# Kernel tuning notes

Measured on AMD Instinct MI355X. Metric: run time of the kernel, lower is better.

The kernel has to match this reference:

```python
import jax, jax.numpy as jnp
import numpy as np

N = 50000      # nodes
E = 800000     # edges (before self-loops)
C_IN = 128
HID = 128
C_OUT = 64
B = 64         # graphs in batch
NEG_SLOPE = 0.2
EPS = 1e-16


def setup_inputs() -> dict:
    key = jax.random.key(0)
    ks = jax.random.split(key, 12)
    x = jax.random.normal(ks[0], (N, C_IN), dtype=jnp.float32)
    edge_index = jax.random.randint(ks[1], (2, E), 0, N, dtype=jnp.int64)
    batch = jnp.sort(jax.random.randint(ks[2], (N,), 0, B, dtype=jnp.int64))
    g1 = 1.0 / np.sqrt(C_IN)
    g2 = 1.0 / np.sqrt(HID)
    return {
        'x': x,
        'edge_index': edge_index,
        'batch': batch,
        'W1': jax.random.normal(ks[3], (C_IN, HID), jnp.float32) * g1,
        'a_src1': jax.random.normal(ks[4], (HID,), jnp.float32) * g2,
        'a_dst1': jax.random.normal(ks[5], (HID,), jnp.float32) * g2,
        'b1': jnp.zeros((HID,), jnp.float32),
        'W2': jax.random.normal(ks[6], (HID, C_OUT), jnp.float32) * g2,
        'a_src2': jax.random.normal(ks[7], (C_OUT,), jnp.float32) / np.sqrt(C_OUT),
        'a_dst2': jax.random.normal(ks[8], (C_OUT,), jnp.float32) / np.sqrt(C_OUT),
        'b2': jnp.zeros((C_OUT,), jnp.float32),
    }


def _gat_conv(x, src, dst, W, a_src, a_dst, b):
    # PyG GATConv, heads=1, self-loops already appended to (src, dst).
    h = x @ W                                   # [N, F]
    alpha = h[src] @ a_src + h[dst] @ a_dst     # [E'] per-edge logit
    alpha = jax.nn.leaky_relu(alpha, NEG_SLOPE)
    # segment softmax over incoming edges of each destination node
    amax = jax.ops.segment_max(alpha, dst, num_segments=N)
    e = jnp.exp(alpha - amax[dst])
    denom = jax.ops.segment_sum(e, dst, num_segments=N)
    att = e / (denom[dst] + EPS)                # [E']
    out = jax.ops.segment_sum(att[:, None] * h[src], dst, num_segments=N)
    return out + b


def reference(x, edge_index, batch, W1, a_src1, a_dst1, b1, W2, a_src2, a_dst2, b2):
    loop = jnp.arange(N, dtype=edge_index.dtype)
    src = jnp.concatenate([edge_index[0], loop])  # add_self_loops=True
    dst = jnp.concatenate([edge_index[1], loop])
    h = _gat_conv(x, src, dst, W1, a_src1, a_dst1, b1)
    h = jax.nn.relu(h)
    h = _gat_conv(h, src, dst, W2, a_src2, a_dst2, b2)
    # global mean pool over graph ids
    sums = jax.ops.segment_sum(h, batch, num_segments=B)          # [B, C_OUT]
    cnt = jax.ops.segment_sum(jnp.ones((N,), h.dtype), batch, num_segments=B)
    pooled = sums / jnp.maximum(cnt, 1.0)[:, None]
    return jax.nn.log_softmax(pooled, axis=1)
```

## Files before the change

### kernel.cpp

```cpp
#include <hip/hip_runtime.h>
#include <math.h>

#define NN 50000
#define EE 800000
#define EP (EE + NN)
#define COUT 64
#define BB 64
#define NEG_SLOPE 0.2f
#define EPSF 1e-16f
#define NPART 8
#define PNODES (NN / NPART)
#define CAPE 128
#define GM 782

typedef unsigned short u16;
typedef __attribute__((ext_vector_type(8))) short bf16x8;
typedef __attribute__((ext_vector_type(4))) float f32x4;

__device__ __forceinline__ u16 f2b(float f) {
    union { float f; unsigned u; } v; v.f = f;
    unsigned u = v.u;
    return (u16)((u + 0x7FFFu + ((u >> 16) & 1u)) >> 16);
}
__device__ __forceinline__ float b2f(u16 h) {
    union { unsigned u; float f; } v; v.u = ((unsigned)h) << 16;
    return v.f;
}
__device__ __forceinline__ float leaky(float v) {
    return (v > 0.f) ? v : NEG_SLOPE * v;
}

__global__ __launch_bounds__(256) void k_pre(const float* __restrict__ W1,
                                             const float* __restrict__ W2,
                                             u16* __restrict__ W1t,
                                             u16* __restrict__ W2t,
                                             int* __restrict__ deg,
                                             float* __restrict__ sums) {
    int b = blockIdx.x;
    if (b < 96) {
        int t = b * 256 + threadIdx.x;
        if (t < 128 * 128) {
            int c = t >> 7, k = t & 127;
            W1t[t] = f2b(W1[k * 128 + c]);
        } else {
            int o = t - 128 * 128;
            int c = o >> 7, k = o & 127;
            W2t[o] = f2b(W2[k * 64 + c]);
        }
    } else {
        int n = (b - 96) * 256 + threadIdx.x;
        if (n < NN) deg[n] = 0;
        if (n < BB * COUT) sums[n] = 0.f;
    }
}

__global__ __launch_bounds__(256) void k_scatter(const int* __restrict__ src,
                                                 const int* __restrict__ dst,
                                                 int* __restrict__ deg,
                                                 u16* __restrict__ col_ell) {
    int v = blockIdx.x & (NPART - 1);
    int cid = blockIdx.x >> 3;
    int nchunk = gridDim.x >> 3;
    int lo = v * PNODES, hi = lo + PNODES;
    for (int e = cid * 256 + threadIdx.x; e < EP; e += nchunk * 256) {
        int dd = (e < EE) ? dst[e] : (e - EE);
        if (dd >= lo && dd < hi) {
            int s = (e < EE) ? src[e] : dd;
            int pos = atomicAdd(&deg[dd], 1);
            if (pos < CAPE) col_ell[(size_t)dd * CAPE + pos] = (u16)s;
        }
    }
}

template <int F, bool ABF16>
__device__ __forceinline__ void gemm_body(int bx,
                                          const void* __restrict__ Xv,
                                          const u16* __restrict__ Wt,
                                          u16* __restrict__ H,
                                          const float* __restrict__ a_src,
                                          const float* __restrict__ a_dst,
                                          float* __restrict__ sdot,
                                          float* __restrict__ ddot) {
    __shared__ u16 Ab[64 * 128];
    __shared__ u16 Bb[F * 128];
    int tid = threadIdx.x;
    int row0 = bx * 64;

    if (ABF16) {
        const u16* X = (const u16*)Xv;
        #pragma unroll
        for (int it = 0; it < 4; it++) {
            int c = it * 256 + tid;
            int row = c >> 4;
            int k8 = (c & 15) * 8;
            int grow = row0 + row;
            uint4 val = {0u, 0u, 0u, 0u};
            if (grow < NN) val = *(const uint4*)&X[(size_t)grow * 128 + k8];
            *(uint4*)&Ab[row * 128 + (k8 ^ ((row & 7) << 3))] = val;
        }
    } else {
        const float* X = (const float*)Xv;
        #pragma unroll
        for (int it = 0; it < 8; it++) {
            int c = it * 256 + tid;
            int e = c * 4;
            int row = e >> 7;
            int col = e & 127;
            int grow = row0 + row;
            float4 v = {0.f, 0.f, 0.f, 0.f};
            if (grow < NN) v = *(const float4*)&X[(size_t)grow * 128 + col];
            ushort4 o;
            o.x = f2b(v.x); o.y = f2b(v.y); o.z = f2b(v.z); o.w = f2b(v.w);
            *(ushort4*)&Ab[row * 128 + (col ^ ((row & 7) << 3))] = o;
        }
    }
    const int NB = F * 128 / 8 / 256;
    #pragma unroll
    for (int it = 0; it < NB; it++) {
        int c = it * 256 + tid;
        int col = c >> 4;
        int k8 = (c & 15) * 8;
        uint4 val = *(const uint4*)&Wt[col * 128 + k8];
        *(uint4*)&Bb[col * 128 + (k8 ^ ((col & 7) << 3))] = val;
    }
    __syncthreads();

    int w = tid >> 6, l = tid & 63;
    int g = l >> 4;
    int rA = l & 15;
    const int NT = F / 16;
    f32x4 acc[NT];
    #pragma unroll
    for (int ct = 0; ct < NT; ct++) {
        acc[ct][0] = 0.f; acc[ct][1] = 0.f; acc[ct][2] = 0.f; acc[ct][3] = 0.f;
    }
    int arow = w * 16 + rA;
    int abase = arow * 128;
    int sw = (rA & 7) << 3;
    #pragma unroll
    for (int ks = 0; ks < 4; ks++) {
        int koff = ks * 32 + g * 8;
        bf16x8 af = *(const bf16x8*)&Ab[abase + (koff ^ sw)];
        #pragma unroll
        for (int ct = 0; ct < NT; ct++) {
            int bcol = ct * 16 + rA;
            bf16x8 bfv = *(const bf16x8*)&Bb[bcol * 128 + (koff ^ sw)];
            acc[ct] = __builtin_amdgcn_mfma_f32_16x16x32_bf16(af, bfv, acc[ct], 0, 0, 0);
        }
    }

    float asv[NT], adv[NT];
    #pragma unroll
    for (int ct = 0; ct < NT; ct++) {
        asv[ct] = a_src[ct * 16 + rA];
        adv[ct] = a_dst[ct * 16 + rA];
    }
    float ps[4] = {0.f, 0.f, 0.f, 0.f};
    float pd[4] = {0.f, 0.f, 0.f, 0.f};
    #pragma unroll
    for (int ct = 0; ct < NT; ct++) {
        #pragma unroll
        for (int r = 0; r < 4; r++) {
            ps[r] += acc[ct][r] * asv[ct];
            pd[r] += acc[ct][r] * adv[ct];
        }
    }
    #pragma unroll
    for (int r = 0; r < 4; r++) {
        int grow = row0 + w * 16 + g * 4 + r;
        if (grow < NN) {
            #pragma unroll
            for (int ct = 0; ct < NT; ct++) {
                H[(size_t)grow * F + ct * 16 + rA] = f2b(acc[ct][r]);
            }
        }
    }
    #pragma unroll
    for (int r = 0; r < 4; r++) {
        #pragma unroll
        for (int off = 1; off < 16; off <<= 1) {
            ps[r] += __shfl_xor(ps[r], off);
            pd[r] += __shfl_xor(pd[r], off);
        }
    }
    if (rA == 0) {
        #pragma unroll
        for (int r = 0; r < 4; r++) {
            int grow = row0 + w * 16 + g * 4 + r;
            if (grow < NN) { sdot[grow] = ps[r]; ddot[grow] = pd[r]; }
        }
    }
}

__global__ __launch_bounds__(256) void k_gemm1(const float* __restrict__ x,
                                               const u16* __restrict__ W1t,
                                               u16* __restrict__ h1,
                                               const float* __restrict__ as1,
                                               const float* __restrict__ ad1,
                                               float* __restrict__ s1,
                                               float* __restrict__ d1) {
    gemm_body<128, false>(blockIdx.x, x, W1t, h1, as1, ad1, s1, d1);
}

__global__ __launch_bounds__(256) void k_gemm2(const u16* __restrict__ x2,
                                               const u16* __restrict__ W2t,
                                               u16* __restrict__ h2,
                                               const float* __restrict__ as2,
                                               const float* __restrict__ ad2,
                                               float* __restrict__ s2,
                                               float* __restrict__ d2) {
    gemm_body<64, true>(blockIdx.x, x2, W2t, h2, as2, ad2, s2, d2);
}

template <int ROWB>
__device__ __forceinline__ float stage_weights(const u16* __restrict__ colrow,
                                               const float* __restrict__ s,
                                               float dn, int deg, int lane,
                                               float* __restrict__ wl,
                                               int* __restrict__ wc) {
    float M = -INFINITY;
    for (int e0 = 0; e0 < deg; e0 += 64) {
        int e = e0 + lane;
        float l = -INFINITY; int c = 0;
        if (e < deg) { c = colrow[e]; l = leaky(s[c] + dn); }
        wl[e0 + lane] = l;
        wc[e0 + lane] = c * ROWB;
        float cm = l;
        #pragma unroll
        for (int off = 32; off; off >>= 1) cm = fmaxf(cm, __shfl_xor(cm, off));
        M = fmaxf(M, cm);
    }
    float Sl = 0.f;
    for (int i0 = 0; i0 < deg; i0 += 64) {
        float u = __expf(wl[i0 + lane] - M);
        wl[i0 + lane] = u;
        Sl += u;
    }
    #pragma unroll
    for (int off = 32; off; off >>= 1) Sl += __shfl_xor(Sl, off);
    return 1.f / (Sl + EPSF);
}

__global__ __launch_bounds__(256) void k_fused1(const int* __restrict__ degv,
                                                const u16* __restrict__ col_ell,
                                                const float* __restrict__ s,
                                                const float* __restrict__ d,
                                                const u16* __restrict__ H,
                                                const float* __restrict__ bias,
                                                u16* __restrict__ outb) {
    const int F = 128;
    __shared__ float wl[4][CAPE];
    __shared__ int   wc[4][CAPE];
    int w = threadIdx.x >> 6;
    int lane = threadIdx.x & 63;
    int n = blockIdx.x * 4 + w;
    if (n >= NN) return;
    int deg = degv[n];
    if (deg > CAPE) deg = CAPE;
    const u16* colrow = col_ell + (size_t)n * CAPE;
    float dn = d[n];
    const char* Hb = (const char*)H + lane * 4;
    float2 acc = {0.f, 0.f};

    float invS = stage_weights<F * 2>(colrow, s, dn, deg, lane, wl[w], wc[w]);
    int i = 0;
    for (; i + 8 <= deg; i += 8) {
        float u0 = wl[w][i+0], u1 = wl[w][i+1], u2 = wl[w][i+2], u3 = wl[w][i+3];
        float u4 = wl[w][i+4], u5 = wl[w][i+5], u6 = wl[w][i+6], u7 = wl[w][i+7];
        int o0 = wc[w][i+0], o1 = wc[w][i+1], o2 = wc[w][i+2], o3 = wc[w][i+3];
        int o4 = wc[w][i+4], o5 = wc[w][i+5], o6 = wc[w][i+6], o7 = wc[w][i+7];
        ushort2 r0 = *(const ushort2*)(Hb + o0);
        ushort2 r1 = *(const ushort2*)(Hb + o1);
        ushort2 r2 = *(const ushort2*)(Hb + o2);
        ushort2 r3 = *(const ushort2*)(Hb + o3);
        ushort2 r4 = *(const ushort2*)(Hb + o4);
        ushort2 r5 = *(const ushort2*)(Hb + o5);
        ushort2 r6 = *(const ushort2*)(Hb + o6);
        ushort2 r7 = *(const ushort2*)(Hb + o7);
        acc.x += u0 * b2f(r0.x); acc.y += u0 * b2f(r0.y);
        acc.x += u1 * b2f(r1.x); acc.y += u1 * b2f(r1.y);
        acc.x += u2 * b2f(r2.x); acc.y += u2 * b2f(r2.y);
        acc.x += u3 * b2f(r3.x); acc.y += u3 * b2f(r3.y);
        acc.x += u4 * b2f(r4.x); acc.y += u4 * b2f(r4.y);
        acc.x += u5 * b2f(r5.x); acc.y += u5 * b2f(r5.y);
        acc.x += u6 * b2f(r6.x); acc.y += u6 * b2f(r6.y);
        acc.x += u7 * b2f(r7.x); acc.y += u7 * b2f(r7.y);
    }
    for (; i < deg; ++i) {
        float u = wl[w][i];
        ushort2 r = *(const ushort2*)(Hb + wc[w][i]);
        acc.x += u * b2f(r.x); acc.y += u * b2f(r.y);
    }
    float2 b = *(const float2*)&bias[lane * 2];
    acc.x = fmaxf(acc.x * invS + b.x, 0.f);
    acc.y = fmaxf(acc.y * invS + b.y, 0.f);
    ushort2 o; o.x = f2b(acc.x); o.y = f2b(acc.y);
    *(ushort2*)&outb[(size_t)n * F + lane * 2] = o;
}

#define NPW 4
__global__ __launch_bounds__(256) void k_fused2(const int* __restrict__ degv,
                                                const u16* __restrict__ col_ell,
                                                const float* __restrict__ s,
                                                const float* __restrict__ d,
                                                const u16* __restrict__ H,
                                                const float* __restrict__ bias,
                                                const int* __restrict__ batch,
                                                float* __restrict__ sums) {
    const int F = 64;
    __shared__ float wl[4][CAPE];
    __shared__ int   wc[4][CAPE];
    int wave = threadIdx.x >> 6;
    int lane = threadIdx.x & 63;
    int base = (blockIdx.x * 4 + wave) * NPW;
    int lim = base + NPW;
    float bs = bias[lane];
    const char* Hb = (const char*)H + lane * 2;
    float gacc = 0.f;
    int gb = batch[base];

    for (int n = base; n < lim; ++n) {
        int b = batch[n];
        if (b != gb) {
            atomicAdd(&sums[gb * COUT + lane], gacc);
            gacc = 0.f; gb = b;
        }
        int deg = degv[n];
        if (deg > CAPE) deg = CAPE;
        const u16* colrow = col_ell + (size_t)n * CAPE;
        float dn = d[n];
        float acc = 0.f;

        float invS = stage_weights<F * 2>(colrow, s, dn, deg, lane, wl[wave], wc[wave]);
        int i = 0;
        for (; i + 8 <= deg; i += 8) {
            float u0 = wl[wave][i+0], u1 = wl[wave][i+1], u2 = wl[wave][i+2], u3 = wl[wave][i+3];
            float u4 = wl[wave][i+4], u5 = wl[wave][i+5], u6 = wl[wave][i+6], u7 = wl[wave][i+7];
            int o0 = wc[wave][i+0], o1 = wc[wave][i+1], o2 = wc[wave][i+2], o3 = wc[wave][i+3];
            int o4 = wc[wave][i+4], o5 = wc[wave][i+5], o6 = wc[wave][i+6], o7 = wc[wave][i+7];
            u16 r0 = *(const u16*)(Hb + o0); u16 r1 = *(const u16*)(Hb + o1);
            u16 r2 = *(const u16*)(Hb + o2); u16 r3 = *(const u16*)(Hb + o3);
            u16 r4 = *(const u16*)(Hb + o4); u16 r5 = *(const u16*)(Hb + o5);
            u16 r6 = *(const u16*)(Hb + o6); u16 r7 = *(const u16*)(Hb + o7);
            acc += u0 * b2f(r0) + u1 * b2f(r1) + u2 * b2f(r2) + u3 * b2f(r3);
            acc += u4 * b2f(r4) + u5 * b2f(r5) + u6 * b2f(r6) + u7 * b2f(r7);
        }
        for (; i < deg; ++i) {
            acc += wl[wave][i] * b2f(*(const u16*)(Hb + wc[wave][i]));
        }
        gacc += acc * invS + bs;
    }
    atomicAdd(&sums[gb * COUT + lane], gacc);
}

__global__ __launch_bounds__(256) void k_logsm(const float* __restrict__ sums,
                                               const int* __restrict__ batch,
                                               float* __restrict__ out) {
    int wave = threadIdx.x >> 6;
    int lane = threadIdx.x & 63;
    int g = blockIdx.x * 4 + wave;
    if (g >= BB) return;
    int lo = 0, hi = NN;
    while (lo < hi) { int mid = (lo + hi) >> 1; if (batch[mid] < g) lo = mid + 1; else hi = mid; }
    int l2 = lo, h2 = NN;
    while (l2 < h2) { int mid = (l2 + h2) >> 1; if (batch[mid] < g + 1) l2 = mid + 1; else h2 = mid; }
    float cnt = (float)(h2 - lo);
    float mean = sums[g * COUT + lane] / fmaxf(cnt, 1.f);
    float mx = mean;
    #pragma unroll
    for (int off = 32; off; off >>= 1) mx = fmaxf(mx, __shfl_xor(mx, off));
    float ex = __expf(mean - mx);
    float sm = ex;
    #pragma unroll
    for (int off = 32; off; off >>= 1) sm += __shfl_xor(sm, off);
    out[g * COUT + lane] = mean - mx - logf(sm);
}

extern "C" void kernel_launch(void* const* d_in, const int* in_sizes, int n_in,
                              void* d_out, int out_size, void* d_ws, size_t ws_size,
                              hipStream_t stream) {
    const float* x      = (const float*)d_in[0];
    const int*   eidx   = (const int*)d_in[1];
    const int*   batch  = (const int*)d_in[2];
    const float* W1     = (const float*)d_in[3];
    const float* a_src1 = (const float*)d_in[4];
    const float* a_dst1 = (const float*)d_in[5];
    const float* b1     = (const float*)d_in[6];
    const float* W2     = (const float*)d_in[7];
    const float* a_src2 = (const float*)d_in[8];
    const float* a_dst2 = (const float*)d_in[9];
    const float* b2     = (const float*)d_in[10];
    float* out = (float*)d_out;

    const int* src = eidx;
    const int* dst = eidx + EE;

    char* w = (char*)d_ws;
    auto alloc = [&](size_t bytes) { void* p = (void*)w; w += (bytes + 255) & ~(size_t)255; return p; };
    float* sums  = (float*)alloc((size_t)BB * COUT * 4);
    float* s1    = (float*)alloc((size_t)NN * 4);
    float* d1    = (float*)alloc((size_t)NN * 4);
    float* s2    = (float*)alloc((size_t)NN * 4);
    float* d2    = (float*)alloc((size_t)NN * 4);
    int* deg     = (int*)alloc((size_t)NN * 4);
    u16* col_ell = (u16*)alloc((size_t)NN * CAPE * 2);
    u16* h1      = (u16*)alloc((size_t)NN * 128 * 2);
    u16* x2      = (u16*)alloc((size_t)NN * 128 * 2);
    u16* h2      = (u16*)alloc((size_t)NN * 64 * 2);
    u16* W1t     = (u16*)alloc((size_t)128 * 128 * 2);
    u16* W2t     = (u16*)alloc((size_t)64 * 128 * 2);

    dim3 blk(256);
    int gN4 = (NN + 3) / 4;

    k_pre<<<292, blk, 0, stream>>>(W1, W2, W1t, W2t, deg, sums);
    k_scatter<<<4096, blk, 0, stream>>>(src, dst, deg, col_ell);

    k_gemm1<<<GM, blk, 0, stream>>>(x, W1t, h1, a_src1, a_dst1, s1, d1);
    k_fused1<<<gN4, blk, 0, stream>>>(deg, col_ell, s1, d1, h1, b1, x2);

    k_gemm2<<<GM, blk, 0, stream>>>(x2, W2t, h2, a_src2, a_dst2, s2, d2);
    k_fused2<<<NN / (4 * NPW), blk, 0, stream>>>(deg, col_ell, s2, d2, h2, b2, batch, sums);

    k_logsm<<<(BB + 3) / 4, blk, 0, stream>>>(sums, batch, out);
}
```

Before: 150.3 us.

## Split layer-1 attention into weight kernel and channel-sliced gather kernel

Layer-1 aggregation is split in two. A new kernel computes the normalized softmax weights per edge and stores them as bf16 in an ELL array. The gather kernel then runs four times as many blocks, each handling a 32-channel slice with four edge groups per wave, and reduces the partial sums with shuffles. This is meant to increase parallelism and memory-level parallelism in the gather. The cost is an extra launch, extra global traffic for the weight array, and bf16 rounding of the attention weights.

Result: slower. 190.6 us (+26.9%).

```diff
diff --git a/kernel.cpp b/kernel.cpp
--- a/kernel.cpp
+++ b/kernel.cpp
@@ -12,6 +12,7 @@
 #define PNODES (NN / NPART)
 #define CAPE 128
 #define GM 782
+#define NSL 4
 
 typedef unsigned short u16;
 typedef __attribute__((ext_vector_type(8))) short bf16x8;
@@ -25,6 +26,12 @@
 __device__ __forceinline__ float b2f(u16 h) {
     union { unsigned u; float f; } v; v.u = ((unsigned)h) << 16;
     return v.f;
+}
+__device__ __forceinline__ float lo16(unsigned v) {
+    union { unsigned u; float f; } x; x.u = v << 16; return x.f;
+}
+__device__ __forceinline__ float hi16(unsigned v) {
+    union { unsigned u; float f; } x; x.u = v & 0xffff0000u; return x.f;
 }
 __device__ __forceinline__ float leaky(float v) {
     return (v > 0.f) ? v : NEG_SLOPE * v;
@@ -212,6 +219,105 @@
     gemm_body<64, true>(blockIdx.x, x2, W2t, h2, as2, ad2, s2, d2);
 }
 
+__global__ __launch_bounds__(256) void k_weights(const int* __restrict__ degv,
+                                                 const u16* __restrict__ col_ell,
+                                                 const float* __restrict__ s,
+                                                 const float* __restrict__ d,
+                                                 u16* __restrict__ w_ell) {
+    __shared__ float wl[4][CAPE];
+    int w = threadIdx.x >> 6;
+    int lane = threadIdx.x & 63;
+    int n = blockIdx.x * 4 + w;
+    int deg = degv[n];
+    if (deg > CAPE) deg = CAPE;
+    const u16* colrow = col_ell + (size_t)n * CAPE;
+    float dn = d[n];
+
+    float M = -INFINITY;
+    for (int e0 = 0; e0 < deg; e0 += 64) {
+        int e = e0 + lane;
+        float l = -INFINITY;
+        if (e < deg) l = leaky(s[colrow[e]] + dn);
+        wl[w][e0 + lane] = l;
+        float cm = l;
+        #pragma unroll
+        for (int off = 32; off; off >>= 1) cm = fmaxf(cm, __shfl_xor(cm, off));
+        M = fmaxf(M, cm);
+    }
+    float Sl = 0.f;
+    for (int i0 = 0; i0 < deg; i0 += 64) {
+        float u = __expf(wl[w][i0 + lane] - M);
+        wl[w][i0 + lane] = u;
+        Sl += u;
+    }
+    #pragma unroll
+    for (int off = 32; off; off >>= 1) Sl += __shfl_xor(Sl, off);
+    float invS = 1.f / (Sl + EPSF);
+
+    int degC = (deg + 63) & ~63;
+    for (int i0 = 0; i0 < degC; i0 += 64) {
+        w_ell[(size_t)n * CAPE + i0 + lane] = f2b(wl[w][i0 + lane] * invS);
+    }
+}
+
+__global__ __launch_bounds__(256) void k_fused1(const int* __restrict__ degv,
+                                                const u16* __restrict__ col_ell,
+                                                const u16* __restrict__ w_ell,
+                                                const u16* __restrict__ H,
+                                                const float* __restrict__ bias,
+                                                u16* __restrict__ outb) {
+    const int F = 128;
+    __shared__ float wl[4][CAPE];
+    __shared__ int   off[4][CAPE];
+    int w = threadIdx.x >> 6;
+    int lane = threadIdx.x & 63;
+    int c = blockIdx.x & (NSL - 1);
+    int n = (blockIdx.x >> 2) * 4 + w;
+    int deg = degv[n];
+    if (deg > CAPE) deg = CAPE;
+    int degR = (deg + 31) & ~31;
+
+    {
+        float wf = (lane < degR) ? b2f(w_ell[(size_t)n * CAPE + lane]) : 0.f;
+        int   of = (lane < deg) ? ((int)col_ell[(size_t)n * CAPE + lane] << 8) : 0;
+        wl[w][lane] = wf;
+        off[w][lane] = of;
+        if (degR > 64) {
+            int e = 64 + lane;
+            wl[w][e] = (e < degR) ? b2f(w_ell[(size_t)n * CAPE + e]) : 0.f;
+            off[w][e] = (e < deg) ? ((int)col_ell[(size_t)n * CAPE + e] << 8) : 0;
+        }
+    }
+
+    int g = lane >> 4;
+    int sub = lane & 15;
+    const char* Hb = (const char*)H + c * 64 + sub * 4;
+    float2 acc = {0.f, 0.f};
+
+    for (int i = 0; i < degR; i += 32) {
+        #pragma unroll
+        for (int j = 0; j < 8; j++) {
+            int e = i + j * 4 + g;
+            float wv = wl[w][e];
+            int   o  = off[w][e];
+            unsigned p = *(const unsigned*)(Hb + o);
+            acc.x += wv * lo16(p);
+            acc.y += wv * hi16(p);
+        }
+    }
+    acc.x += __shfl_xor(acc.x, 16); acc.x += __shfl_xor(acc.x, 32);
+    acc.y += __shfl_xor(acc.y, 16); acc.y += __shfl_xor(acc.y, 32);
+
+    if (g == 0) {
+        int ch = c * 32 + sub * 2;
+        float2 b = *(const float2*)&bias[ch];
+        float ox = fmaxf(acc.x + b.x, 0.f);
+        float oy = fmaxf(acc.y + b.y, 0.f);
+        ushort2 o2; o2.x = f2b(ox); o2.y = f2b(oy);
+        *(ushort2*)&outb[(size_t)n * F + ch] = o2;
+    }
+}
+
 template <int ROWB>
 __device__ __forceinline__ float stage_weights(const u16* __restrict__ colrow,
                                                const float* __restrict__ s,
@@ -239,63 +345,6 @@
     #pragma unroll
     for (int off = 32; off; off >>= 1) Sl += __shfl_xor(Sl, off);
     return 1.f / (Sl + EPSF);
-}
-
-__global__ __launch_bounds__(256) void k_fused1(const int* __restrict__ degv,
-                                                const u16* __restrict__ col_ell,
-                                                const float* __restrict__ s,
-                                                const float* __restrict__ d,
-                                                const u16* __restrict__ H,
-                                                const float* __restrict__ bias,
-                                                u16* __restrict__ outb) {
-    const int F = 128;
-    __shared__ float wl[4][CAPE];
-    __shared__ int   wc[4][CAPE];
-    int w = threadIdx.x >> 6;
-    int lane = threadIdx.x & 63;
-    int n = blockIdx.x * 4 + w;
-    if (n >= NN) return;
-    int deg = degv[n];
-    if (deg > CAPE) deg = CAPE;
-    const u16* colrow = col_ell + (size_t)n * CAPE;
-    float dn = d[n];
-    const char* Hb = (const char*)H + lane * 4;
-    float2 acc = {0.f, 0.f};
-
-    float invS = stage_weights<F * 2>(colrow, s, dn, deg, lane, wl[w], wc[w]);
-    int i = 0;
-    for (; i + 8 <= deg; i += 8) {
-        float u0 = wl[w][i+0], u1 = wl[w][i+1], u2 = wl[w][i+2], u3 = wl[w][i+3];
-        float u4 = wl[w][i+4], u5 = wl[w][i+5], u6 = wl[w][i+6], u7 = wl[w][i+7];
-        int o0 = wc[w][i+0], o1 = wc[w][i+1], o2 = wc[w][i+2], o3 = wc[w][i+3];
-        int o4 = wc[w][i+4], o5 = wc[w][i+5], o6 = wc[w][i+6], o7 = wc[w][i+7];
-        ushort2 r0 = *(const ushort2*)(Hb + o0);
-        ushort2 r1 = *(const ushort2*)(Hb + o1);
-        ushort2 r2 = *(const ushort2*)(Hb + o2);
-        ushort2 r3 = *(const ushort2*)(Hb + o3);
-        ushort2 r4 = *(const ushort2*)(Hb + o4);
-        ushort2 r5 = *(const ushort2*)(Hb + o5);
-        ushort2 r6 = *(const ushort2*)(Hb + o6);
-        ushort2 r7 = *(const ushort2*)(Hb + o7);
-        acc.x += u0 * b2f(r0.x); acc.y += u0 * b2f(r0.y);
-        acc.x += u1 * b2f(r1.x); acc.y += u1 * b2f(r1.y);
-        acc.x += u2 * b2f(r2.x); acc.y += u2 * b2f(r2.y);
-        acc.x += u3 * b2f(r3.x); acc.y += u3 * b2f(r3.y);
-        acc.x += u4 * b2f(r4.x); acc.y += u4 * b2f(r4.y);
-        acc.x += u5 * b2f(r5.x); acc.y += u5 * b2f(r5.y);
-        acc.x += u6 * b2f(r6.x); acc.y += u6 * b2f(r6.y);
-        acc.x += u7 * b2f(r7.x); acc.y += u7 * b2f(r7.y);
-    }
-    for (; i < deg; ++i) {
-        float u = wl[w][i];
-        ushort2 r = *(const ushort2*)(Hb + wc[w][i]);
-        acc.x += u * b2f(r.x); acc.y += u * b2f(r.y);
-    }
-    float2 b = *(const float2*)&bias[lane * 2];
-    acc.x = fmaxf(acc.x * invS + b.x, 0.f);
-    acc.y = fmaxf(acc.y * invS + b.y, 0.f);
-    ushort2 o; o.x = f2b(acc.x); o.y = f2b(acc.y);
-    *(ushort2*)&outb[(size_t)n * F + lane * 2] = o;
 }
 
 #define NPW 4
@@ -404,6 +453,7 @@
     float* d2    = (float*)alloc((size_t)NN * 4);
     int* deg     = (int*)alloc((size_t)NN * 4);
     u16* col_ell = (u16*)alloc((size_t)NN * CAPE * 2);
+    u16* w_ell   = (u16*)alloc((size_t)NN * CAPE * 2);
     u16* h1      = (u16*)alloc((size_t)NN * 128 * 2);
     u16* x2      = (u16*)alloc((size_t)NN * 128 * 2);
     u16* h2      = (u16*)alloc((size_t)NN * 64 * 2);
@@ -417,7 +467,8 @@
     k_scatter<<<4096, blk, 0, stream>>>(src, dst, deg, col_ell);
 
     k_gemm1<<<GM, blk, 0, stream>>>(x, W1t, h1, a_src1, a_dst1, s1, d1);
-    k_fused1<<<gN4, blk, 0, stream>>>(deg, col_ell, s1, d1, h1, b1, x2);
+    k_weights<<<gN4, blk, 0, stream>>>(deg, col_ell, s1, d1, w_ell);
+    k_fused1<<<gN4 * NSL, blk, 0, stream>>>(deg, col_ell, w_ell, h1, b1, x2);
 
     k_gemm2<<<GM, blk, 0, stream>>>(x2, W2t, h2, a_src2, a_dst2, s2, d2);
     k_fused2<<<NN / (4 * NPW), blk, 0, stream>>>(deg, col_ell, s2, d2, h2, b2, batch, sums);
```
